# Kernel optimization log

Measured on AMD Instinct MI355X. Metric: run time of the kernel, lower is better.

## Reference

```python
import jax, jax.numpy as jnp
import numpy as np

N_LAYERS = 4
D_MODEL = 64        # 8*8 hardcoded in source
D_STATE = 128
D_CONV = 4
EXPAND = 2
HEADDIM = 64        # Mamba2Simple default
D_INNER = EXPAND * D_MODEL            # 128
NHEADS = D_INNER // HEADDIM           # 2
NGROUPS = 1
D_IN_PROJ = 2 * D_INNER + 2 * NGROUPS * D_STATE + NHEADS   # 514
CONV_DIM = D_INNER + 2 * NGROUPS * D_STATE                 # 384
EPS = 1e-5
B_SZ, SEQ = 8, 4096


def setup_inputs() -> dict:
    key = jax.random.key(0)
    ks = jax.random.split(key, 8)
    s = 0.02
    x = jax.random.normal(ks[0], (B_SZ, SEQ, D_MODEL), jnp.float32)
    in_proj_w = jax.random.normal(ks[1], (N_LAYERS, D_IN_PROJ, D_MODEL), jnp.float32) * s
    conv_w = jax.random.normal(ks[2], (N_LAYERS, CONV_DIM, 1, D_CONV), jnp.float32) * 0.2
    conv_b = jnp.zeros((N_LAYERS, CONV_DIM), jnp.float32)
    # dt_bias ~ inverse-softplus of small dt values
    dt_bias = jax.random.uniform(ks[3], (N_LAYERS, NHEADS), jnp.float32, -4.0, 0.0)
    A_log = jnp.log(jax.random.uniform(ks[4], (N_LAYERS, NHEADS), jnp.float32, 1.0, 16.0))
    D = jnp.ones((N_LAYERS, NHEADS), jnp.float32)
    norm_w = jnp.ones((N_LAYERS, D_INNER), jnp.float32)
    out_proj_w = jax.random.normal(ks[5], (N_LAYERS, D_MODEL, D_INNER), jnp.float32) * s
    return {"x": x, "in_proj_w": in_proj_w, "conv_w": conv_w, "conv_b": conv_b,
            "dt_bias": dt_bias, "A_log": A_log, "D": D, "norm_w": norm_w,
            "out_proj_w": out_proj_w}


def _ssm(xh, dt, A, Bm, Cm):
    """Selective-scan SSM. xh:(B,L,H,P) dt:(B,L,H) A:(H,) Bm,Cm:(B,L,S) -> (B,L,H,P)"""
    dA = jnp.exp(dt * A)  # (B,L,H)

    def step(h, inp):
        dA_t, dt_t, x_t, B_t, C_t = inp
        # h: (B,H,P,S)
        h = h * dA_t[:, :, None, None] + (dt_t[:, :, None] * x_t)[..., None] * B_t[:, None, None, :]
        y = jnp.einsum('bhps,bs->bhp', h, C_t)
        return h, y

    b = xh.shape[0]
    h0 = jnp.zeros((b, NHEADS, HEADDIM, D_STATE), xh.dtype)
    xs = (jnp.moveaxis(dA, 1, 0), jnp.moveaxis(dt, 1, 0), jnp.moveaxis(xh, 1, 0),
          jnp.moveaxis(Bm, 1, 0), jnp.moveaxis(Cm, 1, 0))
    _, ys = jax.lax.scan(step, h0, xs)
    return jnp.moveaxis(ys, 0, 1)


def _layer(x, p):
    in_w, cw, cb, dtb, Alog, Dp, nw, ow = p
    zxbcdt = x @ in_w.T                                   # (B,L,514)
    z = zxbcdt[..., :D_INNER]
    xBC = zxbcdt[..., D_INNER:D_INNER + CONV_DIM]
    dt = jax.nn.softplus(zxbcdt[..., -NHEADS:] + dtb)     # (B,L,H)
    # causal depthwise conv over sequence
    xc = jnp.moveaxis(xBC, -1, 1)                         # (B,C,L)
    xc = jax.lax.conv_general_dilated(xc, cw, (1,), [(D_CONV - 1, 0)],
                                      dimension_numbers=('NCH', 'OIH', 'NCH'),
                                      feature_group_count=CONV_DIM)
    xBC = jax.nn.silu(jnp.moveaxis(xc + cb[None, :, None], 1, -1))
    xs = xBC[..., :D_INNER]
    Bm = xBC[..., D_INNER:D_INNER + D_STATE]
    Cm = xBC[..., D_INNER + D_STATE:]
    xh = xs.reshape(xs.shape[0], xs.shape[1], NHEADS, HEADDIM)
    A = -jnp.exp(Alog)                                    # (H,)
    y = _ssm(xh, dt, A, Bm, Cm) + Dp[None, None, :, None] * xh
    y = y.reshape(y.shape[0], y.shape[1], D_INNER)
    # gated RMSNorm (norm_before_gate=False): rmsnorm(y * silu(z)) * w
    y = y * jax.nn.silu(z)
    y = y * jax.lax.rsqrt(jnp.mean(y * y, axis=-1, keepdims=True) + EPS) * nw
    return y @ ow.T


def reference(x, in_proj_w, conv_w, conv_b, dt_bias, A_log, D, norm_w, out_proj_w):
    def body(xc, p):
        return _layer(xc, p) + xc, None
    out, _ = jax.lax.scan(body, x, (in_proj_w, conv_w, conv_b, dt_bias, A_log, D, norm_w, out_proj_w))
    return out
```

## Files before the change

kernel.cpp:

```cpp
#include <hip/hip_runtime.h>
#include <math.h>

#define B_SZ 8
#define SEQ  4096
#define DM   64
#define DI   128
#define NH   2
#define HD   64
#define DS   128
#define DIP  514
#define ZW   512
#define CD   384
#define QC   64
#define NC   64
#define NR   (B_SZ*SEQ)

typedef __attribute__((ext_vector_type(8))) short bf16x8;
typedef __attribute__((ext_vector_type(4))) float f32x4;

__device__ __forceinline__ unsigned short f2bf(float f) {
    union { float f; unsigned int u; } x; x.f = f;
    unsigned int r = x.u + 0x7fffu + ((x.u >> 16) & 1u);
    return (unsigned short)(r >> 16);
}
__device__ __forceinline__ float bf2f(unsigned short h) {
    union { unsigned int u; float f; } x; x.u = ((unsigned int)h) << 16;
    return x.f;
}
__device__ __forceinline__ bf16x8 fragld(const unsigned short* base, int r0, int k0, int ld) {
    int l = threadIdx.x & 63;
    return *(const bf16x8*)(base + (size_t)(r0 + (l & 15)) * ld + k0 + (l >> 4) * 8);
}

__global__ __launch_bounds__(256) void k_inproj(const float* __restrict__ X,
                                                const float* __restrict__ W,
                                                unsigned short* __restrict__ ZXb,
                                                float* __restrict__ DT) {
    __shared__ unsigned short As[64][72];
    __shared__ unsigned short Bs[64][72];
    int m0 = blockIdx.x * 64, n0 = blockIdx.y * 64;
    int tid = threadIdx.x;
    int r = tid >> 2, q = tid & 3;
    for (int u = 0; u < 4; u++) {
        int k = q * 16 + u * 4;
        float4 av = *(const float4*)(X + (size_t)(m0 + r) * 64 + k);
        unsigned int p0 = f2bf(av.x) | ((unsigned int)f2bf(av.y) << 16);
        unsigned int p1 = f2bf(av.z) | ((unsigned int)f2bf(av.w) << 16);
        *(uint2*)&As[r][k] = make_uint2(p0, p1);
        int n = n0 + r;
        float4 bv = make_float4(0.f, 0.f, 0.f, 0.f);
        if (n < DIP) bv = *(const float4*)(W + (size_t)n * 64 + k);
        p0 = f2bf(bv.x) | ((unsigned int)f2bf(bv.y) << 16);
        p1 = f2bf(bv.z) | ((unsigned int)f2bf(bv.w) << 16);
        *(uint2*)&Bs[r][k] = make_uint2(p0, p1);
    }
    __syncthreads();
    int wid = tid >> 6, lane = tid & 63;
    int q4 = lane >> 4, c16 = lane & 15;
    int ntMax = (n0 < 512) ? 4 : 1;
    for (int nt = 0; nt < ntMax; nt++) {
        f32x4 acc = {0.f, 0.f, 0.f, 0.f};
        for (int ks = 0; ks < 2; ks++) {
            bf16x8 a = fragld(&As[0][0], wid * 16, ks * 32, 72);
            bf16x8 b = fragld(&Bs[0][0], nt * 16, ks * 32, 72);
            acc = __builtin_amdgcn_mfma_f32_16x16x32_bf16(a, b, acc, 0, 0, 0);
        }
        int n = n0 + nt * 16 + c16;
        if (n < 512) {
            for (int rr = 0; rr < 4; rr++) {
                int m = m0 + wid * 16 + q4 * 4 + rr;
                ZXb[(size_t)m * ZW + n] = f2bf(acc[rr]);
            }
        } else if (n < DIP) {
            for (int rr = 0; rr < 4; rr++) {
                int m = m0 + wid * 16 + q4 * 4 + rr;
                DT[(size_t)m * 2 + (n - 512)] = acc[rr];
            }
        }
    }
}

__global__ __launch_bounds__(512, 4) void k_chunk1(
        const unsigned short* __restrict__ ZXb, const float* __restrict__ DT,
        const float* __restrict__ CW, const float* __restrict__ CB,
        const float* __restrict__ dtb, const float* __restrict__ Alog,
        const float* __restrict__ Dv,
        unsigned short* __restrict__ SL, unsigned short* __restrict__ ECB,
        float* __restrict__ TB, float* __restrict__ YB) {
    __shared__ unsigned short sBt[128][72];
    __shared__ unsigned short sXt[128][72];
    __shared__ unsigned short uBC[2][64][136];
    __shared__ float s_cum[2][64], s_dt[2][64], s_w[2][64], s_e[2][64];
    unsigned short (*sM)[64][72] = (unsigned short (*)[64][72])&uBC[0][0][0];

    int c = blockIdx.x, b = blockIdx.y;
    size_t rbase = (size_t)b * SEQ + c * QC;
    int tid = threadIdx.x;
    int wid = tid >> 6, lane = tid & 63;

    if (wid < 2) {
        int h = wid, j = lane;
        float raw = DT[(rbase + j) * 2 + h] + dtb[h];
        float dt = (raw > 20.f) ? raw : log1pf(__expf(raw));
        float A = -__expf(Alog[h]);
        float x = dt * A;
        for (int off = 1; off < 64; off <<= 1) {
            float o = __shfl_up(x, off);
            if (lane >= off) x += o;
        }
        float T = __shfl(x, 63);
        s_dt[h][j] = dt;
        s_cum[h][j] = x;
        s_w[h][j] = __expf(T - x) * dt;
        s_e[h][j] = __expf(x);
        if (j == 0) TB[(b * 2 + h) * NC + c] = __expf(T);
    }
    __syncthreads();

    size_t ecbase = ((size_t)(b * NC + c)) * 2 * 8192;
    for (int e = tid; e < 64 * 96; e += 512) {
        int j = e / 96;
        int q = e - j * 96;
        int cc = q * 4;
        int l = c * QC + j;
        const unsigned short* zp = ZXb + (rbase + j) * ZW + 128 + cc;
        uint2 a0 = *(const uint2*)zp;
        uint2 a1 = make_uint2(0, 0), a2 = make_uint2(0, 0), a3 = make_uint2(0, 0);
        if (l >= 1) a1 = *(const uint2*)(zp - ZW);
        if (l >= 2) a2 = *(const uint2*)(zp - 2 * ZW);
        if (l >= 3) a3 = *(const uint2*)(zp - 3 * ZW);
        float v[4];
#pragma unroll
        for (int u = 0; u < 4; u++) {
            unsigned int w0 = (u < 2) ? a0.x : a0.y;
            unsigned int w1 = (u < 2) ? a1.x : a1.y;
            unsigned int w2 = (u < 2) ? a2.x : a2.y;
            unsigned int w3 = (u < 2) ? a3.x : a3.y;
            int sh = (u & 1) * 16;
            float r0 = bf2f((unsigned short)(w0 >> sh));
            float r1 = bf2f((unsigned short)(w1 >> sh));
            float r2 = bf2f((unsigned short)(w2 >> sh));
            float r3 = bf2f((unsigned short)(w3 >> sh));
            float4 wv = *(const float4*)(CW + (cc + u) * 4);
            float t = CB[cc + u] + wv.w * r0 + wv.z * r1 + wv.y * r2 + wv.x * r3;
            v[u] = t / (1.f + __expf(-t));
        }
        if (cc < 128) {
#pragma unroll
            for (int u = 0; u < 4; u++) sXt[cc + u][j] = f2bf(v[u]);
        } else if (cc < 256) {
            int s = cc - 128;
            unsigned int p0 = f2bf(v[0]) | ((unsigned int)f2bf(v[1]) << 16);
            unsigned int p1 = f2bf(v[2]) | ((unsigned int)f2bf(v[3]) << 16);
            *(uint2*)&uBC[0][j][s] = make_uint2(p0, p1);
#pragma unroll
            for (int u = 0; u < 4; u++) sBt[s + u][j] = f2bf(v[u]);
        } else {
            int s = cc - 256;
            unsigned int p0 = f2bf(v[0]) | ((unsigned int)f2bf(v[1]) << 16);
            unsigned int p1 = f2bf(v[2]) | ((unsigned int)f2bf(v[3]) << 16);
            *(uint2*)&uBC[1][j][s] = make_uint2(p0, p1);
            float e0 = s_e[0][j], e1 = s_e[1][j];
            unsigned int q0 = f2bf(v[0] * e0) | ((unsigned int)f2bf(v[1] * e0) << 16);
            unsigned int q1 = f2bf(v[2] * e0) | ((unsigned int)f2bf(v[3] * e0) << 16);
            *(uint2*)(ECB + ecbase + (size_t)j * 128 + s) = make_uint2(q0, q1);
            q0 = f2bf(v[0] * e1) | ((unsigned int)f2bf(v[1] * e1) << 16);
            q1 = f2bf(v[2] * e1) | ((unsigned int)f2bf(v[3] * e1) << 16);
            *(uint2*)(ECB + ecbase + 8192 + (size_t)j * 128 + s) = make_uint2(q0, q1);
        }
    }
    __syncthreads();

    int q4 = lane >> 4, c16 = lane & 15;
    f32x4 gacc[2];
    {
#pragma unroll
        for (int u = 0; u < 2; u++) {
            int t = wid * 2 + u;
            int it = t >> 2, jt = t & 3;
            f32x4 acc = {0.f, 0.f, 0.f, 0.f};
            for (int ks = 0; ks < 4; ks++) {
                bf16x8 a = fragld(&uBC[1][0][0], it * 16, ks * 32, 136);
                bf16x8 bb = fragld(&uBC[0][0][0], jt * 16, ks * 32, 136);
                acc = __builtin_amdgcn_mfma_f32_16x16x32_bf16(a, bb, acc, 0, 0, 0);
            }
            gacc[u] = acc;
        }
    }
    __syncthreads();
#pragma unroll
    for (int u = 0; u < 2; u++) {
        int t = wid * 2 + u;
        int it = t >> 2, jt = t & 3;
        int j = jt * 16 + c16;
        for (int rr = 0; rr < 4; rr++) {
            int i = it * 16 + q4 * 4 + rr;
            float gv = gacc[u][rr];
            for (int h = 0; h < 2; h++) {
                float m = 0.f;
                if (j <= i) m = gv * __expf(s_cum[h][i] - s_cum[h][j]) * s_dt[h][j];
                sM[h][i][j] = f2bf(m);
            }
        }
    }
    __syncthreads();

#pragma unroll
    for (int u = 0; u < 4; u++) {
        int idx = wid * 4 + u;
        int h = idx >> 4, tt = idx & 15;
        int it = tt >> 2, pt = tt & 3;
        float dco = Dv[h];
        int pg = h * 64 + pt * 16 + c16;
        f32x4 acc;
        for (int rr = 0; rr < 4; rr++) {
            int i = it * 16 + q4 * 4 + rr;
            acc[rr] = dco * bf2f(sXt[pg][i]);
        }
        for (int ks = 0; ks < 2; ks++) {
            bf16x8 a = fragld(&sM[h][0][0], it * 16, ks * 32, 72);
            bf16x8 bb = fragld(&sXt[0][0], h * 64 + pt * 16, ks * 32, 72);
            acc = __builtin_amdgcn_mfma_f32_16x16x32_bf16(a, bb, acc, 0, 0, 0);
        }
        for (int rr = 0; rr < 4; rr++) {
            int i = it * 16 + q4 * 4 + rr;
            YB[(rbase + i) * DI + pg] = acc[rr];
        }
    }
    size_t slbase = ((size_t)(b * NC + c)) * 16384;
#pragma unroll
    for (int u = 0; u < 8; u++) {
        int idx = wid * 8 + u;
        int ptl = idx >> 3, st = idx & 7;
        int h = ptl >> 2;
        f32x4 acc = {0.f, 0.f, 0.f, 0.f};
        for (int ks = 0; ks < 2; ks++) {
            int jb = ks * 32 + (lane >> 4) * 8;
            bf16x8 a = fragld(&sXt[0][0], ptl * 16, ks * 32, 72);
            bf16x8 aw;
#pragma unroll
            for (int t = 0; t < 8; t++) aw[t] = (short)f2bf(bf2f((unsigned short)a[t]) * s_w[h][jb + t]);
            bf16x8 bb = fragld(&sBt[0][0], st * 16, ks * 32, 72);
            acc = __builtin_amdgcn_mfma_f32_16x16x32_bf16(aw, bb, acc, 0, 0, 0);
        }
        int s = st * 16 + c16;
        for (int rr = 0; rr < 4; rr++) {
            int p = ptl * 16 + q4 * 4 + rr;
            float vv = acc[rr];
            float vn = __shfl_xor(vv, 1);
            if (!(lane & 1)) {
                unsigned int pk = f2bf(vv) | ((unsigned int)f2bf(vn) << 16);
                *(unsigned int*)(SL + slbase + (size_t)p * 128 + s) = pk;
            }
        }
    }
}

__global__ __launch_bounds__(256) void k_scan(unsigned short* __restrict__ SL,
                                              const float* __restrict__ TB) {
    int bid = blockIdx.x;
    int b = bid >> 6;
    int ps = (bid & 63) * 256 + threadIdx.x;
    int h = ps >> 13;
    const float* dAp = TB + (b * 2 + h) * NC;
    size_t base = (size_t)(b * NC) * 16384 + ps;
    float hacc = 0.f;
#pragma unroll 8
    for (int cc = 0; cc < NC; cc++) {
        size_t idx = base + (size_t)cc * 16384;
        float slv = bf2f(SL[idx]);
        SL[idx] = f2bf(hacc);
        hacc = hacc * dAp[cc] + slv;
    }
}

__global__ __launch_bounds__(512) void k_chunk2(const unsigned short* __restrict__ SL,
                                                const unsigned short* __restrict__ ECB,
                                                float* __restrict__ YB) {
    __shared__ unsigned short sH[128][136];
    __shared__ unsigned short sE[128][136];
    int c = blockIdx.x, b = blockIdx.y;
    size_t rbase = (size_t)b * SEQ + c * QC;
    int tid = threadIdx.x;
    size_t base = ((size_t)(b * NC + c)) * 16384;
    for (int u = 0; u < 4; u++) {
        int e = u * 512 + tid;
        int row = e >> 4, cb8 = (e & 15) * 8;
        *(uint4*)&sH[row][cb8] = *(const uint4*)(SL + base + (size_t)row * 128 + cb8);
        *(uint4*)&sE[row][cb8] = *(const uint4*)(ECB + base + (size_t)row * 128 + cb8);
    }
    __syncthreads();
    int wid = tid >> 6, lane = tid & 63;
    int q4 = lane >> 4, c16 = lane & 15;
#pragma unroll
    for (int u = 0; u < 4; u++) {
        int idx = wid * 4 + u;
        int h = idx >> 4, tt = idx & 15;
        int it = tt >> 2, pt = tt & 3;
        f32x4 acc = {0.f, 0.f, 0.f, 0.f};
        for (int ks = 0; ks < 4; ks++) {
            bf16x8 a = fragld(&sE[0][0], h * 64 + it * 16, ks * 32, 136);
            bf16x8 bb = fragld(&sH[0][0], h * 64 + pt * 16, ks * 32, 136);
            acc = __builtin_amdgcn_mfma_f32_16x16x32_bf16(a, bb, acc, 0, 0, 0);
        }
        int pg = h * 64 + pt * 16 + c16;
        for (int rr = 0; rr < 4; rr++) {
            int i = it * 16 + q4 * 4 + rr;
            size_t o = (rbase + i) * DI + pg;
            YB[o] += acc[rr];
        }
    }
}

__global__ __launch_bounds__(256) void k_out(const float* __restrict__ YB,
                                             const unsigned short* __restrict__ ZXb,
                                             const float* __restrict__ NW,
                                             const float* __restrict__ OW,
                                             float* __restrict__ XR) {
    __shared__ unsigned short sG[64][136];
    __shared__ unsigned short sW[64][136];
    int tid = threadIdx.x;
    size_t rbase = (size_t)blockIdx.x * 64;
    for (int u = 0; u < 8; u++) {
        int e4 = (u * 256 + tid) * 4;
        int m = e4 >> 7, d = e4 & 127;
        float4 v = *(const float4*)(OW + e4);
        unsigned int p0 = f2bf(v.x) | ((unsigned int)f2bf(v.y) << 16);
        unsigned int p1 = f2bf(v.z) | ((unsigned int)f2bf(v.w) << 16);
        *(uint2*)&sW[m][d] = make_uint2(p0, p1);
    }
    {
        int row = tid >> 2, part = tid & 3;
        int d0 = part * 32;
        size_t yo = (rbase + row) * DI + d0;
        const unsigned short* zp = ZXb + (rbase + row) * ZW + d0;
        float zf[32];
        for (int u = 0; u < 4; u++) {
            uint4 zw = *(const uint4*)(zp + u * 8);
            unsigned int ww[4] = {zw.x, zw.y, zw.z, zw.w};
            for (int t = 0; t < 4; t++) {
                zf[u * 8 + t * 2]     = bf2f((unsigned short)(ww[t] & 0xffff));
                zf[u * 8 + t * 2 + 1] = bf2f((unsigned short)(ww[t] >> 16));
            }
        }
        float gv[32];
        float ss = 0.f;
        for (int u = 0; u < 8; u++) {
            float4 y = *(const float4*)(YB + yo + u * 4);
            float z0 = zf[u * 4], z1 = zf[u * 4 + 1], z2 = zf[u * 4 + 2], z3 = zf[u * 4 + 3];
            float g0 = y.x * (z0 / (1.f + __expf(-z0)));
            float g1 = y.y * (z1 / (1.f + __expf(-z1)));
            float g2 = y.z * (z2 / (1.f + __expf(-z2)));
            float g3 = y.w * (z3 / (1.f + __expf(-z3)));
            gv[u * 4 + 0] = g0; gv[u * 4 + 1] = g1; gv[u * 4 + 2] = g2; gv[u * 4 + 3] = g3;
            ss += g0 * g0 + g1 * g1 + g2 * g2 + g3 * g3;
        }
        float o = __shfl_xor(ss, 1); ss += o;
        o = __shfl_xor(ss, 2); ss += o;
        float rms = rsqrtf(ss * (1.f / 128.f) + 1e-5f);
        for (int u = 0; u < 8; u++) {
            int d = d0 + u * 4;
            unsigned int p0 = f2bf(gv[u * 4] * rms * NW[d]) | ((unsigned int)f2bf(gv[u * 4 + 1] * rms * NW[d + 1]) << 16);
            unsigned int p1 = f2bf(gv[u * 4 + 2] * rms * NW[d + 2]) | ((unsigned int)f2bf(gv[u * 4 + 3] * rms * NW[d + 3]) << 16);
            *(uint2*)&sG[row][d] = make_uint2(p0, p1);
        }
    }
    __syncthreads();
    int wid = tid >> 6, lane = tid & 63;
    int q4 = lane >> 4, c16 = lane & 15;
    for (int nt = 0; nt < 4; nt++) {
        f32x4 acc = {0.f, 0.f, 0.f, 0.f};
        for (int ks = 0; ks < 4; ks++) {
            bf16x8 a = fragld(&sG[0][0], wid * 16, ks * 32, 136);
            bf16x8 bb = fragld(&sW[0][0], nt * 16, ks * 32, 136);
            acc = __builtin_amdgcn_mfma_f32_16x16x32_bf16(a, bb, acc, 0, 0, 0);
        }
        int n = nt * 16 + c16;
        for (int rr = 0; rr < 4; rr++) {
            int m = wid * 16 + q4 * 4 + rr;
            XR[(rbase + m) * DM + n] += acc[rr];
        }
    }
}

extern "C" void kernel_launch(void* const* d_in, const int* in_sizes, int n_in,
                              void* d_out, int out_size, void* d_ws, size_t ws_size,
                              hipStream_t stream) {
    const float* x       = (const float*)d_in[0];
    const float* in_w    = (const float*)d_in[1];
    const float* conv_w  = (const float*)d_in[2];
    const float* conv_b  = (const float*)d_in[3];
    const float* dt_bias = (const float*)d_in[4];
    const float* A_log   = (const float*)d_in[5];
    const float* Dp      = (const float*)d_in[6];
    const float* norm_w  = (const float*)d_in[7];
    const float* out_w   = (const float*)d_in[8];
    float* out = (float*)d_out;
    float* ws  = (float*)d_ws;

    float* yb = ws;
    float* dt = yb + (size_t)NR * DI;
    float* tb = dt + (size_t)NR * 2;
    unsigned short* zxb = (unsigned short*)(tb + 1024);
    unsigned short* sl  = zxb + (size_t)NR * ZW;
    unsigned short* ecb = sl + (size_t)B_SZ * NC * 16384;

    hipMemcpyAsync(out, x, (size_t)NR * DM * sizeof(float), hipMemcpyDeviceToDevice, stream);

    for (int layer = 0; layer < 4; layer++) {
        k_inproj<<<dim3(NR / 64, 9), 256, 0, stream>>>(out, in_w + (size_t)layer * DIP * DM, zxb, dt);
        k_chunk1<<<dim3(NC, B_SZ), 512, 0, stream>>>(zxb, dt,
                conv_w + (size_t)layer * CD * 4, conv_b + (size_t)layer * CD,
                dt_bias + layer * NH, A_log + layer * NH, Dp + layer * NH,
                sl, ecb, tb, yb);
        k_scan<<<512, 256, 0, stream>>>(sl, tb);
        k_chunk2<<<dim3(NC, B_SZ), 512, 0, stream>>>(sl, ecb, yb);
        k_out<<<NR / 64, 256, 0, stream>>>(yb, zxb, norm_w + layer * DI, out_w + (size_t)layer * DM * DI, out);
    }
}
```

Before: 399.2 us.

## Fuse chunk2 with output projection, pre-convert weights and activations to bf16

Merges k_chunk2 and k_out into one kernel that adds the inter-chunk contribution, applies the gated RMSNorm and the out projection, then writes the residual and a bf16 copy of the next-layer input. Weights are converted to bf16 once up front, and the intra-chunk Y buffer is stored in bf16. k_inproj now reads pre-converted bf16 X and W straight into registers with a larger 256-row M tile and packed stores. The goal is less global traffic, fewer launches and less repeated conversion work, at the cost of more rounding of Y to bf16 and extra workspace.

```diff
diff --git a/kernel.cpp b/kernel.cpp
--- a/kernel.cpp
+++ b/kernel.cpp
@@ -14,6 +14,7 @@
 #define QC   64
 #define NC   64
 #define NR   (B_SZ*SEQ)
+#define WPAD 576
 
 typedef __attribute__((ext_vector_type(8))) short bf16x8;
 typedef __attribute__((ext_vector_type(4))) float f32x4;
@@ -32,50 +33,83 @@
     return *(const bf16x8*)(base + (size_t)(r0 + (l & 15)) * ld + k0 + (l >> 4) * 8);
 }
 
-__global__ __launch_bounds__(256) void k_inproj(const float* __restrict__ X,
-                                                const float* __restrict__ W,
+__global__ __launch_bounds__(256) void k_wcvt(const float* __restrict__ in_w,
+                                              const float* __restrict__ out_w,
+                                              unsigned short* __restrict__ Wb,
+                                              unsigned short* __restrict__ OWb) {
+    int idx = blockIdx.x * 256 + threadIdx.x;
+    if (idx < 4 * WPAD * 64) {
+        int l = idx / (WPAD * 64), r = idx % (WPAD * 64);
+        int n = r >> 6, k = r & 63;
+        float v = (n < DIP) ? in_w[(size_t)l * DIP * 64 + (size_t)n * 64 + k] : 0.f;
+        Wb[idx] = f2bf(v);
+    }
+    if (idx < 4 * 64 * 128) OWb[idx] = f2bf(out_w[idx]);
+}
+
+__global__ __launch_bounds__(256) void k_xcvt(const float* __restrict__ X,
+                                              unsigned short* __restrict__ Xb) {
+    int idx = (blockIdx.x * 256 + threadIdx.x) * 4;
+    float4 v = *(const float4*)(X + idx);
+    uint2 p;
+    p.x = f2bf(v.x) | ((unsigned int)f2bf(v.y) << 16);
+    p.y = f2bf(v.z) | ((unsigned int)f2bf(v.w) << 16);
+    *(uint2*)(Xb + idx) = p;
+}
+
+__global__ __launch_bounds__(256) void k_inproj(const unsigned short* __restrict__ Xb,
+                                                const unsigned short* __restrict__ Wb,
                                                 unsigned short* __restrict__ ZXb,
                                                 float* __restrict__ DT) {
-    __shared__ unsigned short As[64][72];
-    __shared__ unsigned short Bs[64][72];
-    int m0 = blockIdx.x * 64, n0 = blockIdx.y * 64;
+    int m0 = blockIdx.x * 256;
+    int n0 = blockIdx.y * 64;
     int tid = threadIdx.x;
-    int r = tid >> 2, q = tid & 3;
-    for (int u = 0; u < 4; u++) {
-        int k = q * 16 + u * 4;
-        float4 av = *(const float4*)(X + (size_t)(m0 + r) * 64 + k);
-        unsigned int p0 = f2bf(av.x) | ((unsigned int)f2bf(av.y) << 16);
-        unsigned int p1 = f2bf(av.z) | ((unsigned int)f2bf(av.w) << 16);
-        *(uint2*)&As[r][k] = make_uint2(p0, p1);
-        int n = n0 + r;
-        float4 bv = make_float4(0.f, 0.f, 0.f, 0.f);
-        if (n < DIP) bv = *(const float4*)(W + (size_t)n * 64 + k);
-        p0 = f2bf(bv.x) | ((unsigned int)f2bf(bv.y) << 16);
-        p1 = f2bf(bv.z) | ((unsigned int)f2bf(bv.w) << 16);
-        *(uint2*)&Bs[r][k] = make_uint2(p0, p1);
-    }
-    __syncthreads();
     int wid = tid >> 6, lane = tid & 63;
     int q4 = lane >> 4, c16 = lane & 15;
-    int ntMax = (n0 < 512) ? 4 : 1;
-    for (int nt = 0; nt < ntMax; nt++) {
-        f32x4 acc = {0.f, 0.f, 0.f, 0.f};
-        for (int ks = 0; ks < 2; ks++) {
-            bf16x8 a = fragld(&As[0][0], wid * 16, ks * 32, 72);
-            bf16x8 b = fragld(&Bs[0][0], nt * 16, ks * 32, 72);
-            acc = __builtin_amdgcn_mfma_f32_16x16x32_bf16(a, b, acc, 0, 0, 0);
-        }
-        int n = n0 + nt * 16 + c16;
-        if (n < 512) {
-            for (int rr = 0; rr < 4; rr++) {
-                int m = m0 + wid * 16 + q4 * 4 + rr;
-                ZXb[(size_t)m * ZW + n] = f2bf(acc[rr]);
+    int mb = m0 + wid * 64;
+    bf16x8 af[4][2];
+#pragma unroll
+    for (int mt = 0; mt < 4; mt++)
+#pragma unroll
+        for (int ks = 0; ks < 2; ks++)
+            af[mt][ks] = *(const bf16x8*)(Xb + (size_t)(mb + mt * 16 + c16) * 64 + ks * 32 + q4 * 8);
+    if (n0 < 512) {
+#pragma unroll
+        for (int nt = 0; nt < 4; nt++) {
+            bf16x8 bf[2];
+#pragma unroll
+            for (int ks = 0; ks < 2; ks++)
+                bf[ks] = *(const bf16x8*)(Wb + (size_t)(n0 + nt * 16 + c16) * 64 + ks * 32 + q4 * 8);
+#pragma unroll
+            for (int mt = 0; mt < 4; mt++) {
+                f32x4 acc = {0.f, 0.f, 0.f, 0.f};
+                acc = __builtin_amdgcn_mfma_f32_16x16x32_bf16(af[mt][0], bf[0], acc, 0, 0, 0);
+                acc = __builtin_amdgcn_mfma_f32_16x16x32_bf16(af[mt][1], bf[1], acc, 0, 0, 0);
+#pragma unroll
+                for (int rr = 0; rr < 4; rr++) {
+                    float v = acc[rr];
+                    float vn = __shfl_xor(v, 1);
+                    if (!(lane & 1)) {
+                        unsigned int pk = f2bf(v) | ((unsigned int)f2bf(vn) << 16);
+                        *(unsigned int*)(ZXb + (size_t)(mb + mt * 16 + q4 * 4 + rr) * ZW + n0 + nt * 16 + c16) = pk;
+                    }
+                }
             }
-        } else if (n < DIP) {
-            for (int rr = 0; rr < 4; rr++) {
-                int m = m0 + wid * 16 + q4 * 4 + rr;
-                DT[(size_t)m * 2 + (n - 512)] = acc[rr];
-            }
+        }
+    } else {
+        bf16x8 bf[2];
+#pragma unroll
+        for (int ks = 0; ks < 2; ks++)
+            bf[ks] = *(const bf16x8*)(Wb + (size_t)(512 + c16) * 64 + ks * 32 + q4 * 8);
+#pragma unroll
+        for (int mt = 0; mt < 4; mt++) {
+            f32x4 acc = {0.f, 0.f, 0.f, 0.f};
+            acc = __builtin_amdgcn_mfma_f32_16x16x32_bf16(af[mt][0], bf[0], acc, 0, 0, 0);
+            acc = __builtin_amdgcn_mfma_f32_16x16x32_bf16(af[mt][1], bf[1], acc, 0, 0, 0);
+            if (c16 < 2)
+#pragma unroll
+                for (int rr = 0; rr < 4; rr++)
+                    DT[(size_t)(mb + mt * 16 + q4 * 4 + rr) * 2 + c16] = acc[rr];
         }
     }
 }
@@ -86,7 +120,7 @@
         const float* __restrict__ dtb, const float* __restrict__ Alog,
         const float* __restrict__ Dv,
         unsigned short* __restrict__ SL, unsigned short* __restrict__ ECB,
-        float* __restrict__ TB, float* __restrict__ YB) {
+        float* __restrict__ TB, unsigned short* __restrict__ YBb) {
     __shared__ unsigned short sBt[128][72];
     __shared__ unsigned short sXt[128][72];
     __shared__ unsigned short uBC[2][64][136];
@@ -173,19 +207,17 @@
 
     int q4 = lane >> 4, c16 = lane & 15;
     f32x4 gacc[2];
-    {
-#pragma unroll
-        for (int u = 0; u < 2; u++) {
-            int t = wid * 2 + u;
-            int it = t >> 2, jt = t & 3;
-            f32x4 acc = {0.f, 0.f, 0.f, 0.f};
-            for (int ks = 0; ks < 4; ks++) {
-                bf16x8 a = fragld(&uBC[1][0][0], it * 16, ks * 32, 136);
-                bf16x8 bb = fragld(&uBC[0][0][0], jt * 16, ks * 32, 136);
-                acc = __builtin_amdgcn_mfma_f32_16x16x32_bf16(a, bb, acc, 0, 0, 0);
-            }
-            gacc[u] = acc;
-        }
+#pragma unroll
+    for (int u = 0; u < 2; u++) {
+        int t = wid * 2 + u;
+        int it = t >> 2, jt = t & 3;
+        f32x4 acc = {0.f, 0.f, 0.f, 0.f};
+        for (int ks = 0; ks < 4; ks++) {
+            bf16x8 a = fragld(&uBC[1][0][0], it * 16, ks * 32, 136);
+            bf16x8 bb = fragld(&uBC[0][0][0], jt * 16, ks * 32, 136);
+            acc = __builtin_amdgcn_mfma_f32_16x16x32_bf16(a, bb, acc, 0, 0, 0);
+        }
+        gacc[u] = acc;
     }
     __syncthreads();
 #pragma unroll
@@ -224,7 +256,12 @@
         }
         for (int rr = 0; rr < 4; rr++) {
             int i = it * 16 + q4 * 4 + rr;
-            YB[(rbase + i) * DI + pg] = acc[rr];
+            float v = acc[rr];
+            float vn = __shfl_xor(v, 1);
+            if (!(lane & 1)) {
+                unsigned int pk = f2bf(v) | ((unsigned int)f2bf(vn) << 16);
+                *(unsigned int*)(YBb + (rbase + i) * DI + pg) = pk;
+            }
         }
     }
     size_t slbase = ((size_t)(b * NC + c)) * 16384;
@@ -274,14 +311,20 @@
     }
 }
 
-__global__ __launch_bounds__(512) void k_chunk2(const unsigned short* __restrict__ SL,
-                                                const unsigned short* __restrict__ ECB,
-                                                float* __restrict__ YB) {
-    __shared__ unsigned short sH[128][136];
-    __shared__ unsigned short sE[128][136];
+__global__ __launch_bounds__(512, 2) void k_fused(
+        const unsigned short* __restrict__ SL, const unsigned short* __restrict__ ECB,
+        const unsigned short* __restrict__ YBb, const unsigned short* __restrict__ ZXb,
+        const float* __restrict__ NW, const unsigned short* __restrict__ OWb,
+        float* __restrict__ XR, unsigned short* __restrict__ Xbn) {
+    __shared__ __attribute__((aligned(16))) unsigned short sH[128][136];
+    __shared__ __attribute__((aligned(16))) unsigned short sE[128][136];
+    float* sGf = (float*)&sH[0][0];
+    unsigned short (*sG)[136] = (unsigned short (*)[136])&sE[0][0];
+
     int c = blockIdx.x, b = blockIdx.y;
     size_t rbase = (size_t)b * SEQ + c * QC;
     int tid = threadIdx.x;
+    int wid = tid >> 6, lane = tid & 63;
     size_t base = ((size_t)(b * NC + c)) * 16384;
     for (int u = 0; u < 4; u++) {
         int e = u * 512 + tid;
@@ -290,8 +333,10 @@
         *(uint4*)&sE[row][cb8] = *(const uint4*)(ECB + base + (size_t)row * 128 + cb8);
     }
     __syncthreads();
-    int wid = tid >> 6, lane = tid & 63;
     int q4 = lane >> 4, c16 = lane & 15;
+
+    float yv[4][4];
+    int tit[4], tpg[4];
 #pragma unroll
     for (int u = 0; u < 4; u++) {
         int idx = wid * 4 + u;
@@ -304,81 +349,59 @@
             acc = __builtin_amdgcn_mfma_f32_16x16x32_bf16(a, bb, acc, 0, 0, 0);
         }
         int pg = h * 64 + pt * 16 + c16;
+        tit[u] = it; tpg[u] = pg;
         for (int rr = 0; rr < 4; rr++) {
             int i = it * 16 + q4 * 4 + rr;
-            size_t o = (rbase + i) * DI + pg;
-            YB[o] += acc[rr];
-        }
-    }
-}
-
-__global__ __launch_bounds__(256) void k_out(const float* __restrict__ YB,
-                                             const unsigned short* __restrict__ ZXb,
-                                             const float* __restrict__ NW,
-                                             const float* __restrict__ OW,
-                                             float* __restrict__ XR) {
-    __shared__ unsigned short sG[64][136];
-    __shared__ unsigned short sW[64][136];
-    int tid = threadIdx.x;
-    size_t rbase = (size_t)blockIdx.x * 64;
-    for (int u = 0; u < 8; u++) {
-        int e4 = (u * 256 + tid) * 4;
-        int m = e4 >> 7, d = e4 & 127;
-        float4 v = *(const float4*)(OW + e4);
-        unsigned int p0 = f2bf(v.x) | ((unsigned int)f2bf(v.y) << 16);
-        unsigned int p1 = f2bf(v.z) | ((unsigned int)f2bf(v.w) << 16);
-        *(uint2*)&sW[m][d] = make_uint2(p0, p1);
-    }
+            float y = acc[rr] + bf2f(YBb[(rbase + i) * DI + pg]);
+            float z = bf2f(ZXb[(rbase + i) * ZW + pg]);
+            yv[u][rr] = y * (z / (1.f + __expf(-z)));
+        }
+    }
+    __syncthreads();
+#pragma unroll
+    for (int u = 0; u < 4; u++)
+        for (int rr = 0; rr < 4; rr++) {
+            int i = tit[u] * 16 + q4 * 4 + rr;
+            sGf[i * 132 + tpg[u]] = yv[u][rr];
+        }
+    __syncthreads();
     {
-        int row = tid >> 2, part = tid & 3;
-        int d0 = part * 32;
-        size_t yo = (rbase + row) * DI + d0;
-        const unsigned short* zp = ZXb + (rbase + row) * ZW + d0;
-        float zf[32];
-        for (int u = 0; u < 4; u++) {
-            uint4 zw = *(const uint4*)(zp + u * 8);
-            unsigned int ww[4] = {zw.x, zw.y, zw.z, zw.w};
-            for (int t = 0; t < 4; t++) {
-                zf[u * 8 + t * 2]     = bf2f((unsigned short)(ww[t] & 0xffff));
-                zf[u * 8 + t * 2 + 1] = bf2f((unsigned short)(ww[t] >> 16));
-            }
-        }
-        float gv[32];
+        int row = tid >> 3, p0 = (tid & 7) * 16;
+        float g[16];
         float ss = 0.f;
-        for (int u = 0; u < 8; u++) {
-            float4 y = *(const float4*)(YB + yo + u * 4);
-            float z0 = zf[u * 4], z1 = zf[u * 4 + 1], z2 = zf[u * 4 + 2], z3 = zf[u * 4 + 3];
-            float g0 = y.x * (z0 / (1.f + __expf(-z0)));
-            float g1 = y.y * (z1 / (1.f + __expf(-z1)));
-            float g2 = y.z * (z2 / (1.f + __expf(-z2)));
-            float g3 = y.w * (z3 / (1.f + __expf(-z3)));
-            gv[u * 4 + 0] = g0; gv[u * 4 + 1] = g1; gv[u * 4 + 2] = g2; gv[u * 4 + 3] = g3;
-            ss += g0 * g0 + g1 * g1 + g2 * g2 + g3 * g3;
-        }
-        float o = __shfl_xor(ss, 1); ss += o;
-        o = __shfl_xor(ss, 2); ss += o;
+        for (int t2 = 0; t2 < 16; t2++) { g[t2] = sGf[row * 132 + p0 + t2]; ss += g[t2] * g[t2]; }
+        ss += __shfl_xor(ss, 1);
+        ss += __shfl_xor(ss, 2);
+        ss += __shfl_xor(ss, 4);
         float rms = rsqrtf(ss * (1.f / 128.f) + 1e-5f);
-        for (int u = 0; u < 8; u++) {
-            int d = d0 + u * 4;
-            unsigned int p0 = f2bf(gv[u * 4] * rms * NW[d]) | ((unsigned int)f2bf(gv[u * 4 + 1] * rms * NW[d + 1]) << 16);
-            unsigned int p1 = f2bf(gv[u * 4 + 2] * rms * NW[d + 2]) | ((unsigned int)f2bf(gv[u * 4 + 3] * rms * NW[d + 3]) << 16);
-            *(uint2*)&sG[row][d] = make_uint2(p0, p1);
-        }
-    }
-    __syncthreads();
-    int wid = tid >> 6, lane = tid & 63;
-    int q4 = lane >> 4, c16 = lane & 15;
-    for (int nt = 0; nt < 4; nt++) {
+        for (int t2 = 0; t2 < 16; t2 += 2) {
+            unsigned int pk = f2bf(g[t2] * rms * NW[p0 + t2]) |
+                              ((unsigned int)f2bf(g[t2 + 1] * rms * NW[p0 + t2 + 1]) << 16);
+            *(unsigned int*)&sG[row][p0 + t2] = pk;
+        }
+    }
+    __syncthreads();
+#pragma unroll
+    for (int u = 0; u < 2; u++) {
+        int t = wid * 2 + u;
+        int mt = t >> 2, nt = t & 3;
         f32x4 acc = {0.f, 0.f, 0.f, 0.f};
         for (int ks = 0; ks < 4; ks++) {
-            bf16x8 a = fragld(&sG[0][0], wid * 16, ks * 32, 136);
-            bf16x8 bb = fragld(&sW[0][0], nt * 16, ks * 32, 136);
+            bf16x8 a = fragld(&sG[0][0], mt * 16, ks * 32, 136);
+            bf16x8 bb = *(const bf16x8*)(OWb + (size_t)(nt * 16 + c16) * 128 + ks * 32 + q4 * 8);
             acc = __builtin_amdgcn_mfma_f32_16x16x32_bf16(a, bb, acc, 0, 0, 0);
         }
-        int n = nt * 16 + c16;
-        for (int rr = 0; rr < 4; rr++) {
-            int m = wid * 16 + q4 * 4 + rr;
-            XR[(rbase + m) * DM + n] += acc[rr];
+        for (int rr = 0; rr < 4; rr++) {
+            int m = mt * 16 + q4 * 4 + rr;
+            int n = nt * 16 + c16;
+            size_t o = (rbase + m) * DM + n;
+            float v = XR[o] + acc[rr];
+            XR[o] = v;
+            float vn = __shfl_xor(v, 1);
+            if (!(lane & 1)) {
+                unsigned int pk = f2bf(v) | ((unsigned int)f2bf(vn) << 16);
+                *(unsigned int*)(Xbn + o) = pk;
+            }
         }
     }
 }
@@ -398,23 +421,28 @@
     float* out = (float*)d_out;
     float* ws  = (float*)d_ws;
 
-    float* yb = ws;
-    float* dt = yb + (size_t)NR * DI;
+    float* dt = ws;
     float* tb = dt + (size_t)NR * 2;
     unsigned short* zxb = (unsigned short*)(tb + 1024);
-    unsigned short* sl  = zxb + (size_t)NR * ZW;
+    unsigned short* ybb = zxb + (size_t)NR * ZW;
+    unsigned short* sl  = ybb + (size_t)NR * DI;
     unsigned short* ecb = sl + (size_t)B_SZ * NC * 16384;
-
+    unsigned short* xb  = ecb + (size_t)B_SZ * NC * 16384;
+    unsigned short* wb  = xb + (size_t)NR * DM;
+    unsigned short* owb = wb + (size_t)4 * WPAD * 64;
+
+    k_wcvt<<<(4 * WPAD * 64 + 255) / 256, 256, 0, stream>>>(in_w, out_w, wb, owb);
+    k_xcvt<<<NR * DM / 1024, 256, 0, stream>>>(x, xb);
     hipMemcpyAsync(out, x, (size_t)NR * DM * sizeof(float), hipMemcpyDeviceToDevice, stream);
 
     for (int layer = 0; layer < 4; layer++) {
-        k_inproj<<<dim3(NR / 64, 9), 256, 0, stream>>>(out, in_w + (size_t)layer * DIP * DM, zxb, dt);
+        k_inproj<<<dim3(NR / 256, 9), 256, 0, stream>>>(xb, wb + (size_t)layer * WPAD * 64, zxb, dt);
         k_chunk1<<<dim3(NC, B_SZ), 512, 0, stream>>>(zxb, dt,
                 conv_w + (size_t)layer * CD * 4, conv_b + (size_t)layer * CD,
                 dt_bias + layer * NH, A_log + layer * NH, Dp + layer * NH,
-                sl, ecb, tb, yb);
+                sl, ecb, tb, ybb);
         k_scan<<<512, 256, 0, stream>>>(sl, tb);
-        k_chunk2<<<dim3(NC, B_SZ), 512, 0, stream>>>(sl, ecb, yb);
-        k_out<<<NR / 64, 256, 0, stream>>>(yb, zxb, norm_w + layer * DI, out_w + (size_t)layer * DM * DI, out);
-    }
-}
+        k_fused<<<dim3(NC, B_SZ), 512, 0, stream>>>(sl, ecb, ybb, zxb,
+                norm_w + layer * DI, owb + (size_t)layer * 64 * 128, out, xb);
+    }
+}
```

New measurement: 384.8 us. 3.6% less time.
